# Performance work log

Measured on AMD Instinct MI355X. Metric: run time of the kernel, lower is better.

## Reference

```python
import jax, jax.numpy as jnp
import numpy as np

ALPHA = 1.0  # module hardcodes self.alpha = 1.0


def _normalize(m):
    # torch: diag(rowsum^-0.5) @ m @ diag(rowsum^-0.5) == broadcast row/col scaling
    r_inv = jnp.sum(m, axis=0) ** -0.5  # [V]
    return m * r_inv[:, None] * r_inv[None, :]


def setup_inputs() -> dict:
    key = jax.random.key(0)
    k1, k2, k3, k4 = jax.random.split(key, 4)
    V, D_IN, D_OUT, A, B = 2048, 64, 64, 8, 8
    adj = jax.random.uniform(k1, (V, V), dtype=jnp.float32)
    x = jax.random.normal(k2, (A, B, V, D_IN), dtype=jnp.float32)
    # xavier_normal_ on [D_IN, D_OUT]
    std = float(np.sqrt(2.0 / (D_IN + D_OUT)))
    weight = jax.random.normal(k3, (D_IN, D_OUT), dtype=jnp.float32) * std
    bias = jax.random.normal(k4, (D_OUT,), dtype=jnp.float32)
    return {"adj": adj, "x": x, "weight": weight, "bias": bias}


def reference(adj, x, weight, bias):
    # dropout is identity in eval mode
    adj_norm = _normalize(adj)
    sqr_norm = _normalize(adj @ adj)  # computed as in the original (alpha=1 zeroes it)
    m_norm = ALPHA * adj_norm + (1.0 - ALPHA) * sqr_norm  # [V, V]
    x_tmp = jnp.einsum('abvd,de->abve', x, weight)        # project features
    x_out = jnp.einsum('vj,abvd->abjd', m_norm, x_tmp)    # aggregate over nodes
    x_out = x_out + bias
    return jax.nn.relu(x_out)
```

## Files before the change

### kernel.cpp

```cpp
#include <hip/hip_runtime.h>
#include <cstddef>

typedef unsigned short u16;
typedef u16 u16x8 __attribute__((ext_vector_type(8)));
typedef __bf16 bf16x8 __attribute__((ext_vector_type(8)));
typedef float f32x4 __attribute__((ext_vector_type(4)));

static constexpr int V  = 2048;
static constexpr int DD = 64;

__device__ __forceinline__ u16 f2b(float f) {
  union { float f; unsigned int i; } x; x.f = f;
  return (u16)((x.i + 0x7fffu + ((x.i >> 16) & 1u)) >> 16);
}

__device__ __forceinline__ void gll16(const void* g, void* l) {
  __builtin_amdgcn_global_load_lds(
      (const __attribute__((address_space(1))) void*)g,
      (__attribute__((address_space(3))) void*)l, 16, 0, 0);
}

__global__ __launch_bounds__(256) void k_part(const float* __restrict__ adj,
                                              float* __restrict__ partial) {
  int t = threadIdx.x;
  int r0 = blockIdx.x * 16;
  int c0 = t * 8;
  float acc[8] = {0.f, 0.f, 0.f, 0.f, 0.f, 0.f, 0.f, 0.f};
  for (int r = 0; r < 16; ++r) {
    const float4* p = (const float4*)(adj + (size_t)(r0 + r) * V + c0);
    float4 a0 = p[0], a1 = p[1];
    acc[0] += a0.x; acc[1] += a0.y; acc[2] += a0.z; acc[3] += a0.w;
    acc[4] += a1.x; acc[5] += a1.y; acc[6] += a1.z; acc[7] += a1.w;
  }
  #pragma unroll
  for (int k = 0; k < 8; ++k) partial[(size_t)blockIdx.x * V + c0 + k] = acc[k];
}

__global__ __launch_bounds__(256) void k_rinv(const float* __restrict__ partial,
                                              float* __restrict__ rinv) {
  int c = blockIdx.x * 256 + threadIdx.x;
  float s = 0.f;
  for (int i = 0; i < 128; ++i) s += partial[(size_t)i * V + c];
  rinv[c] = rsqrtf(s);
}

__global__ __launch_bounds__(256) void k_tn(const float* __restrict__ adj,
                                            const float* __restrict__ rinv,
                                            u16* __restrict__ At) {
  __shared__ float T[64][65];
  int t = threadIdx.x;
  int v0 = blockIdx.x * 64;
  int j0 = blockIdx.y * 64;
  #pragma unroll
  for (int it = 0; it < 2; ++it) {
    int f = t + it * 256;
    int row = f >> 3;
    int cc = (f & 7) * 8;
    float rv = rinv[v0 + row];
    const float4* p = (const float4*)(adj + (size_t)(v0 + row) * V + j0 + cc);
    float4 a0 = p[0], a1 = p[1];
    T[row][cc + 0] = a0.x * rv; T[row][cc + 1] = a0.y * rv;
    T[row][cc + 2] = a0.z * rv; T[row][cc + 3] = a0.w * rv;
    T[row][cc + 4] = a1.x * rv; T[row][cc + 5] = a1.y * rv;
    T[row][cc + 6] = a1.z * rv; T[row][cc + 7] = a1.w * rv;
  }
  __syncthreads();
  #pragma unroll
  for (int it = 0; it < 2; ++it) {
    int f = t + it * 256;
    int jr = f >> 3;
    int vc = (f & 7) * 8;
    float rj = rinv[j0 + jr];
    u16x8 o;
    #pragma unroll
    for (int k = 0; k < 8; ++k) o[k] = f2b(T[vc + k][jr] * rj);
    *(u16x8*)(At + (size_t)(j0 + jr) * V + v0 + vc) = o;
  }
}

__global__ __launch_bounds__(256) void k_proj(const float* __restrict__ x,
                                              const float* __restrict__ w,
                                              u16* __restrict__ Yt) {
  __shared__ float XL[64][65];
  __shared__ float WL[64][64];
  int t = threadIdx.x;
  int ab = blockIdx.x >> 5;
  int v0 = (blockIdx.x & 31) * 64;
  const float* xb = x + ((size_t)ab * V + v0) * DD;
  #pragma unroll
  for (int it = 0; it < 2; ++it) {
    int f = t + it * 256;
    int row = f >> 3;
    int cc = (f & 7) * 8;
    const float4* px = (const float4*)(xb + f * 8);
    const float4* pw = (const float4*)(w + f * 8);
    float4 x0 = px[0], x1 = px[1];
    float4 w0 = pw[0], w1 = pw[1];
    XL[row][cc + 0] = x0.x; XL[row][cc + 1] = x0.y;
    XL[row][cc + 2] = x0.z; XL[row][cc + 3] = x0.w;
    XL[row][cc + 4] = x1.x; XL[row][cc + 5] = x1.y;
    XL[row][cc + 6] = x1.z; XL[row][cc + 7] = x1.w;
    WL[row][cc + 0] = w0.x; WL[row][cc + 1] = w0.y;
    WL[row][cc + 2] = w0.z; WL[row][cc + 3] = w0.w;
    WL[row][cc + 4] = w1.x; WL[row][cc + 5] = w1.y;
    WL[row][cc + 6] = w1.z; WL[row][cc + 7] = w1.w;
  }
  __syncthreads();
  int v = t & 63;
  int g = t >> 6;
  float acc[16];
  #pragma unroll
  for (int e = 0; e < 16; ++e) acc[e] = 0.f;
  for (int d = 0; d < 64; ++d) {
    float xv = XL[v][d];
    #pragma unroll
    for (int e = 0; e < 16; ++e) acc[e] += xv * WL[d][g * 16 + e];
  }
  __syncthreads();
  #pragma unroll
  for (int e = 0; e < 16; ++e) XL[g * 16 + e][v] = acc[e];
  __syncthreads();
  #pragma unroll
  for (int it = 0; it < 2; ++it) {
    int f = t + it * 256;
    int er = f >> 3;
    int vc = (f & 7) * 8;
    u16x8 o;
    #pragma unroll
    for (int k = 0; k < 8; ++k) o[k] = f2b(XL[er][vc + k]);
    *(u16x8*)(Yt + (size_t)(ab * 64 + er) * V + v0 + vc) = o;
  }
}

#define BM 128
#define BN 128
#define BK 32

__global__ __launch_bounds__(256) void k_gemm(const u16* __restrict__ At,
                                              const u16* __restrict__ Yt,
                                              const float* __restrict__ bias,
                                              float* __restrict__ out) {
  __shared__ u16 Al[BM * BK];
  __shared__ u16 Bl[BN * BK];
  int t = threadIdx.x;
  int m0 = blockIdx.x * BM;
  int n0 = blockIdx.y * BN;
  int lane = t & 63;
  int wave = t >> 6;
  int wm = (wave & 1) * 64;
  int wn = (wave >> 1) * 64;
  int q = lane >> 4;
  int r = lane & 15;

  const f32x4 vzero = {0.f, 0.f, 0.f, 0.f};
  f32x4 acc[4][4];
  #pragma unroll
  for (int i = 0; i < 4; ++i)
    #pragma unroll
    for (int j = 0; j < 4; ++j) acc[i][j] = vzero;

  int eo0 = t * 8;
  int eo1 = (256 + t) * 8;
  int row0 = eo0 >> 5, col0 = eo0 & 31;
  int row1 = eo1 >> 5, col1 = eo1 & 31;

  for (int k0 = 0; k0 < V; k0 += BK) {
    __syncthreads();
    gll16(At + (size_t)(m0 + row0) * V + k0 + col0, Al + eo0);
    gll16(At + (size_t)(m0 + row1) * V + k0 + col1, Al + eo1);
    gll16(Yt + (size_t)(n0 + row0) * V + k0 + col0, Bl + eo0);
    gll16(Yt + (size_t)(n0 + row1) * V + k0 + col1, Bl + eo1);
    __syncthreads();
    bf16x8 a[4], b[4];
    #pragma unroll
    for (int i = 0; i < 4; ++i)
      a[i] = __builtin_bit_cast(bf16x8, *(const u16x8*)(Al + (wm + i * 16 + r) * BK + q * 8));
    #pragma unroll
    for (int j = 0; j < 4; ++j)
      b[j] = __builtin_bit_cast(bf16x8, *(const u16x8*)(Bl + (wn + j * 16 + r) * BK + q * 8));
    #pragma unroll
    for (int i = 0; i < 4; ++i)
      #pragma unroll
      for (int j = 0; j < 4; ++j)
        acc[i][j] = __builtin_amdgcn_mfma_f32_16x16x32_bf16(a[i], b[j], acc[i][j], 0, 0, 0);
  }

  #pragma unroll
  for (int j = 0; j < 4; ++j) {
    int n = n0 + wn + j * 16 + r;
    int e = n & 63;
    int ab = n >> 6;
    float bv = bias[e];
    float* ob = out + (size_t)ab * (V * DD);
    #pragma unroll
    for (int i = 0; i < 4; ++i) {
      #pragma unroll
      for (int reg = 0; reg < 4; ++reg) {
        int jj = m0 + wm + i * 16 + q * 4 + reg;
        ob[(size_t)jj * DD + e] = fmaxf(acc[i][j][reg] + bv, 0.f);
      }
    }
  }
}

extern "C" void kernel_launch(void* const* d_in, const int* in_sizes, int n_in,
                              void* d_out, int out_size, void* d_ws, size_t ws_size,
                              hipStream_t stream) {
  const float* adj  = (const float*)d_in[0];
  const float* x    = (const float*)d_in[1];
  const float* w    = (const float*)d_in[2];
  const float* bias = (const float*)d_in[3];
  float* out = (float*)d_out;

  char* ws = (char*)d_ws;
  u16*   At      = (u16*)ws;
  u16*   Yt      = (u16*)(ws + ((size_t)8 << 20));
  float* partial = (float*)(ws + ((size_t)8 << 20));
  float* rinv    = (float*)(ws + ((size_t)9 << 20));

  k_part<<<128, 256, 0, stream>>>(adj, partial);
  k_rinv<<<8, 256, 0, stream>>>(partial, rinv);
  k_tn<<<dim3(32, 32), 256, 0, stream>>>(adj, rinv, At);
  k_proj<<<2048, 256, 0, stream>>>(x, w, Yt);
  k_gemm<<<dim3(16, 32), 256, 0, stream>>>(At, Yt, bias, out);
}
```

Baseline: 173.0 us.

## Use MFMA for feature projection and deepen GEMM K-step to four panels

```diff
diff --git a/kernel.cpp b/kernel.cpp
--- a/kernel.cpp
+++ b/kernel.cpp
@@ -81,67 +81,82 @@
 __global__ __launch_bounds__(256) void k_proj(const float* __restrict__ x,
                                               const float* __restrict__ w,
                                               u16* __restrict__ Yt) {
-  __shared__ float XL[64][65];
-  __shared__ float WL[64][64];
-  int t = threadIdx.x;
-  int ab = blockIdx.x >> 5;
-  int v0 = (blockIdx.x & 31) * 64;
-  const float* xb = x + ((size_t)ab * V + v0) * DD;
-  #pragma unroll
-  for (int it = 0; it < 2; ++it) {
-    int f = t + it * 256;
-    int row = f >> 3;
-    int cc = (f & 7) * 8;
-    const float4* px = (const float4*)(xb + f * 8);
-    const float4* pw = (const float4*)(w + f * 8);
-    float4 x0 = px[0], x1 = px[1];
-    float4 w0 = pw[0], w1 = pw[1];
-    XL[row][cc + 0] = x0.x; XL[row][cc + 1] = x0.y;
-    XL[row][cc + 2] = x0.z; XL[row][cc + 3] = x0.w;
-    XL[row][cc + 4] = x1.x; XL[row][cc + 5] = x1.y;
-    XL[row][cc + 6] = x1.z; XL[row][cc + 7] = x1.w;
-    WL[row][cc + 0] = w0.x; WL[row][cc + 1] = w0.y;
-    WL[row][cc + 2] = w0.z; WL[row][cc + 3] = w0.w;
-    WL[row][cc + 4] = w1.x; WL[row][cc + 5] = w1.y;
-    WL[row][cc + 6] = w1.z; WL[row][cc + 7] = w1.w;
+  __shared__ u16 WT[64 * 72];
+  int t = threadIdx.x;
+  int ab = blockIdx.x >> 4;
+  int v0 = (blockIdx.x & 15) * 128;
+
+  {
+    const float4* pw = (const float4*)(w + t * 16);
+    float4 c0 = pw[0], c1 = pw[1], c2 = pw[2], c3 = pw[3];
+    float vals[16] = {c0.x, c0.y, c0.z, c0.w, c1.x, c1.y, c1.z, c1.w,
+                      c2.x, c2.y, c2.z, c2.w, c3.x, c3.y, c3.z, c3.w};
+    #pragma unroll
+    for (int k = 0; k < 16; ++k) {
+      int idx = t * 16 + k;
+      WT[(idx & 63) * 72 + (idx >> 6)] = f2b(vals[k]);
+    }
   }
   __syncthreads();
-  int v = t & 63;
-  int g = t >> 6;
-  float acc[16];
-  #pragma unroll
-  for (int e = 0; e < 16; ++e) acc[e] = 0.f;
-  for (int d = 0; d < 64; ++d) {
-    float xv = XL[v][d];
-    #pragma unroll
-    for (int e = 0; e < 16; ++e) acc[e] += xv * WL[d][g * 16 + e];
-  }
-  __syncthreads();
-  #pragma unroll
-  for (int e = 0; e < 16; ++e) XL[g * 16 + e][v] = acc[e];
-  __syncthreads();
-  #pragma unroll
-  for (int it = 0; it < 2; ++it) {
-    int f = t + it * 256;
-    int er = f >> 3;
-    int vc = (f & 7) * 8;
-    u16x8 o;
-    #pragma unroll
-    for (int k = 0; k < 8; ++k) o[k] = f2b(XL[er][vc + k]);
-    *(u16x8*)(Yt + (size_t)(ab * 64 + er) * V + v0 + vc) = o;
-  }
+
+  int lane = t & 63, wave = t >> 6;
+  int q = lane >> 4, r = lane & 15;
+  int vbase = v0 + wave * 32;
+
+  bf16x8 a[4][2];
+  #pragma unroll
+  for (int i = 0; i < 4; ++i)
+    #pragma unroll
+    for (int kk = 0; kk < 2; ++kk)
+      a[i][kk] = __builtin_bit_cast(bf16x8,
+          *(const u16x8*)(WT + (i * 16 + r) * 72 + kk * 32 + q * 8));
+
+  const f32x4 vzero = {0.f, 0.f, 0.f, 0.f};
+  f32x4 acc[4][2];
+  #pragma unroll
+  for (int i = 0; i < 4; ++i) { acc[i][0] = vzero; acc[i][1] = vzero; }
+
+  #pragma unroll
+  for (int nt = 0; nt < 2; ++nt) {
+    int v = vbase + nt * 16 + r;
+    const float* xp = x + ((size_t)ab * V + v) * DD;
+    #pragma unroll
+    for (int kk = 0; kk < 2; ++kk) {
+      const float4* p = (const float4*)(xp + kk * 32 + q * 8);
+      float4 b0 = p[0], b1 = p[1];
+      u16x8 bu;
+      bu[0] = f2b(b0.x); bu[1] = f2b(b0.y); bu[2] = f2b(b0.z); bu[3] = f2b(b0.w);
+      bu[4] = f2b(b1.x); bu[5] = f2b(b1.y); bu[6] = f2b(b1.z); bu[7] = f2b(b1.w);
+      bf16x8 bf = __builtin_bit_cast(bf16x8, bu);
+      #pragma unroll
+      for (int i = 0; i < 4; ++i)
+        acc[i][nt] = __builtin_amdgcn_mfma_f32_16x16x32_bf16(a[i][kk], bf, acc[i][nt], 0, 0, 0);
+    }
+  }
+
+  #pragma unroll
+  for (int i = 0; i < 4; ++i)
+    #pragma unroll
+    for (int nt = 0; nt < 2; ++nt) {
+      int v = vbase + nt * 16 + r;
+      #pragma unroll
+      for (int reg = 0; reg < 4; ++reg) {
+        int e = i * 16 + q * 4 + reg;
+        Yt[(size_t)(ab * 64 + e) * V + v] = f2b(acc[i][nt][reg]);
+      }
+    }
 }
 
 #define BM 128
 #define BN 128
-#define BK 32
+#define PANEL (128 * 32)
 
 __global__ __launch_bounds__(256) void k_gemm(const u16* __restrict__ At,
                                               const u16* __restrict__ Yt,
                                               const float* __restrict__ bias,
                                               float* __restrict__ out) {
-  __shared__ u16 Al[BM * BK];
-  __shared__ u16 Bl[BN * BK];
+  __shared__ u16 Al[4 * PANEL];
+  __shared__ u16 Bl[4 * PANEL];
   int t = threadIdx.x;
   int m0 = blockIdx.x * BM;
   int n0 = blockIdx.y * BN;
@@ -164,25 +179,34 @@
   int row0 = eo0 >> 5, col0 = eo0 & 31;
   int row1 = eo1 >> 5, col1 = eo1 & 31;
 
-  for (int k0 = 0; k0 < V; k0 += BK) {
+  for (int k0 = 0; k0 < V; k0 += 128) {
     __syncthreads();
-    gll16(At + (size_t)(m0 + row0) * V + k0 + col0, Al + eo0);
-    gll16(At + (size_t)(m0 + row1) * V + k0 + col1, Al + eo1);
-    gll16(Yt + (size_t)(n0 + row0) * V + k0 + col0, Bl + eo0);
-    gll16(Yt + (size_t)(n0 + row1) * V + k0 + col1, Bl + eo1);
+    #pragma unroll
+    for (int p = 0; p < 4; ++p) {
+      int kp = k0 + p * 32;
+      gll16(At + (size_t)(m0 + row0) * V + kp + col0, Al + p * PANEL + eo0);
+      gll16(At + (size_t)(m0 + row1) * V + kp + col1, Al + p * PANEL + eo1);
+      gll16(Yt + (size_t)(n0 + row0) * V + kp + col0, Bl + p * PANEL + eo0);
+      gll16(Yt + (size_t)(n0 + row1) * V + kp + col1, Bl + p * PANEL + eo1);
+    }
     __syncthreads();
-    bf16x8 a[4], b[4];
-    #pragma unroll
-    for (int i = 0; i < 4; ++i)
-      a[i] = __builtin_bit_cast(bf16x8, *(const u16x8*)(Al + (wm + i * 16 + r) * BK + q * 8));
-    #pragma unroll
-    for (int j = 0; j < 4; ++j)
-      b[j] = __builtin_bit_cast(bf16x8, *(const u16x8*)(Bl + (wn + j * 16 + r) * BK + q * 8));
-    #pragma unroll
-    for (int i = 0; i < 4; ++i)
+    #pragma unroll
+    for (int p = 0; p < 4; ++p) {
+      bf16x8 a[4], b[4];
+      #pragma unroll
+      for (int i = 0; i < 4; ++i)
+        a[i] = __builtin_bit_cast(bf16x8,
+            *(const u16x8*)(Al + p * PANEL + (wm + i * 16 + r) * 32 + q * 8));
       #pragma unroll
       for (int j = 0; j < 4; ++j)
-        acc[i][j] = __builtin_amdgcn_mfma_f32_16x16x32_bf16(a[i], b[j], acc[i][j], 0, 0, 0);
+        b[j] = __builtin_bit_cast(bf16x8,
+            *(const u16x8*)(Bl + p * PANEL + (wn + j * 16 + r) * 32 + q * 8));
+      #pragma unroll
+      for (int i = 0; i < 4; ++i)
+        #pragma unroll
+        for (int j = 0; j < 4; ++j)
+          acc[i][j] = __builtin_amdgcn_mfma_f32_16x16x32_bf16(a[i], b[j], acc[i][j], 0, 0, 0);
+    }
   }
 
   #pragma unroll
@@ -221,6 +245,6 @@
   k_part<<<128, 256, 0, stream>>>(adj, partial);
   k_rinv<<<8, 256, 0, stream>>>(partial, rinv);
   k_tn<<<dim3(32, 32), 256, 0, stream>>>(adj, rinv, At);
-  k_proj<<<2048, 256, 0, stream>>>(x, w, Yt);
+  k_proj<<<1024, 256, 0, stream>>>(x, w, Yt);
   k_gemm<<<dim3(16, 32), 256, 0, stream>>>(At, Yt, bias, out);
 }
```

New measurement: 153.7 us. -11.1%, faster.
